# Kernel optimization log

Hardware: AMD Instinct MI355X
Metric: run time of the kernel (lower is better)

## Reference

```python
import jax, jax.numpy as jnp
import numpy as np

D_MODEL = 512
NUM_HEADS = 8
D_K = D_MODEL // NUM_HEADS
LN_EPS = 1e-5


def setup_inputs() -> dict:
    key = jax.random.key(0)
    ks = jax.random.split(key, 11)
    d = D_MODEL
    s = 1.0 / np.sqrt(d)
    return {
        "x": jax.random.normal(ks[0], (4, 2048, d), dtype=jnp.float32),
        "Wq": jax.random.uniform(ks[1], (d, d), jnp.float32, -s, s),
        "bq": jax.random.uniform(ks[2], (d,), jnp.float32, -s, s),
        "Wk": jax.random.uniform(ks[3], (d, d), jnp.float32, -s, s),
        "bk": jax.random.uniform(ks[4], (d,), jnp.float32, -s, s),
        "Wv": jax.random.uniform(ks[5], (d, d), jnp.float32, -s, s),
        "bv": jax.random.uniform(ks[6], (d,), jnp.float32, -s, s),
        "Wo": jax.random.uniform(ks[7], (d, d), jnp.float32, -s, s),
        "bo": jax.random.uniform(ks[8], (d,), jnp.float32, -s, s),
        "gamma": jnp.ones((d,), jnp.float32),
        "beta": jnp.zeros((d,), jnp.float32),
    }


def reference(x, Wq, bq, Wk, bk, Wv, bv, Wo, bo, gamma, beta):
    # x: (B, S, D). Dropout is identity (eval mode).
    B, S, D = x.shape
    H, dk = NUM_HEADS, D_K
    # Linear layers use torch convention: y = x @ W.T + b
    q = (x @ Wq.T + bq).reshape(B, S, H, dk).transpose(0, 2, 1, 3)  # (B,H,S,dk)
    k = (x @ Wk.T + bk).reshape(B, S, H, dk).transpose(0, 2, 1, 3)
    v = (x @ Wv.T + bv).reshape(B, S, H, dk).transpose(0, 2, 1, 3)
    scores = jnp.einsum("bhqd,bhkd->bhqk", q, k) / jnp.sqrt(jnp.float32(dk))
    attn = jax.nn.softmax(scores, axis=-1)
    ctx = jnp.einsum("bhqk,bhkd->bhqd", attn, v)  # (B,H,S,dk)
    ctx = ctx.transpose(0, 2, 1, 3).reshape(B, S, D)
    out = ctx @ Wo.T + bo
    # residual + LayerNorm
    y = x + out
    mu = jnp.mean(y, axis=-1, keepdims=True)
    var = jnp.mean(jnp.square(y - mu), axis=-1, keepdims=True)
    return (y - mu) / jnp.sqrt(var + LN_EPS) * gamma + beta
```

## Files before the change

### kernel.cpp

```cpp
#include <hip/hip_runtime.h>
#include <math.h>

#define D 512
#define NH 8
#define DK 64
#define S 2048
#define BATCH 4
#define N_TOK (BATCH * S)

#define QSCALE 0.18033688f

typedef __bf16 bf16x8 __attribute__((ext_vector_type(8)));
typedef __bf16 bf16x4 __attribute__((ext_vector_type(4)));
typedef float f32x4 __attribute__((ext_vector_type(4)));
typedef unsigned int u32x4 __attribute__((ext_vector_type(4)));

#define AS1 __attribute__((address_space(1)))
#define AS3 __attribute__((address_space(3)))

#define OFF_XB   0
#define OFF_WB   8388608
#define OFF_Q    10485760
#define OFF_K    18874368
#define OFF_VT   27262976
#define OFF_CTX  35651584
#define OFF_FLAG 44040192

static __device__ __forceinline__ bf16x8 ldg8(const __bf16* p) {
    return *(const bf16x8*)p;
}
static __device__ __forceinline__ f32x4 mfma16(bf16x8 a, bf16x8 b, f32x4 c) {
    return __builtin_amdgcn_mfma_f32_16x16x32_bf16(a, b, c, 0, 0, 0);
}
static __device__ __forceinline__ float ldf(const void* p, size_t i, int isf) {
    return isf ? ((const float*)p)[i] : (float)(((const __bf16*)p)[i]);
}
static __device__ __forceinline__ float fexp2(float x) {
#if __has_builtin(__builtin_amdgcn_exp2f)
    return __builtin_amdgcn_exp2f(x);
#else
    return exp2f(x);
#endif
}
static __device__ __forceinline__ unsigned pack_trunc(float e0, float e1) {
    return (__builtin_bit_cast(unsigned, e0) >> 16)
         | (__builtin_bit_cast(unsigned, e1) & 0xFFFF0000u);
}
static __device__ __forceinline__ void gload_lds16(const void* g, void* l) {
    __builtin_amdgcn_global_load_lds((const AS1 char*)g, (AS3 char*)l, 16, 0, 0);
}

__global__ __launch_bounds__(256)
void cvt_kernel(const void* __restrict__ x,  const void* __restrict__ Wq,
                const void* __restrict__ Wk, const void* __restrict__ Wv,
                const void* __restrict__ Wo, __bf16* __restrict__ xb,
                __bf16* __restrict__ Wb, int* __restrict__ flag)
{
    const bf16x8 probe = ldg8((const __bf16*)x + (threadIdx.x & 63) * 8);
    int bad = 0;
#pragma unroll
    for (int j = 0; j < 8; ++j) bad |= !(fabsf((float)probe[j]) <= 64.0f);
    const int isf = __any(bad) ? 1 : 0;
    if (blockIdx.x == 0 && threadIdx.x == 0) *flag = isf;

    const size_t i0 = ((size_t)blockIdx.x * 256 + threadIdx.x) * 8;
    const void* src;
    __bf16* dst;
    size_t off;
    if (i0 < 4194304) {
        src = x; off = i0; dst = xb + i0;
    } else {
        const size_t wrel = i0 - 4194304;
        const size_t w = wrel >> 18;
        src = (w == 0) ? Wq : (w == 1) ? Wk : (w == 2) ? Wv : Wo;
        off = wrel & 262143;
        dst = Wb + wrel;
    }
    bf16x8 r;
    if (isf) {
        const float* f = (const float*)src + off;
#pragma unroll
        for (int j = 0; j < 8; ++j) r[j] = (__bf16)f[j];
    } else {
        r = *(const bf16x8*)((const __bf16*)src + off);
    }
    *(bf16x8*)dst = r;
}

__global__ __launch_bounds__(256)
void qkv_kernel(const __bf16* __restrict__ xb, const __bf16* __restrict__ Wb,
                const void* __restrict__ bq, const void* __restrict__ bk,
                const void* __restrict__ bv, const int* __restrict__ flag,
                __bf16* __restrict__ Q, __bf16* __restrict__ K,
                __bf16* __restrict__ Vt)
{
    __shared__ __align__(16) char smem[32768];

    const int isf = *flag;
    const int tid = threadIdx.x;
    const int w = tid >> 6, l = tid & 63;
    const int lane16 = l & 15, quad = l >> 4;
    const int wm = w >> 1, wn = w & 1;
    const int m0 = blockIdx.x * 128;
    const int by = blockIdx.y;
    const int n0 = by * 128;

    const int cwl = w * 64 + l;
    const int g0 = (cwl & 3) ^ ((cwl >> 3) & 3);
    const __bf16* aS0 = xb + (size_t)(m0 + (cwl >> 2)) * D + g0 * 8;
    const __bf16* aS1 = aS0 + (size_t)64 * D;
    const __bf16* bS0 = Wb + (size_t)(n0 + (cwl >> 2)) * D + g0 * 8;
    const __bf16* bS1 = bS0 + (size_t)64 * D;

    const int sw = (quad ^ ((lane16 >> 1) & 3)) * 16;
    const int aoff = (wm * 64 + lane16) * 64 + sw;
    const int boff = 8192 + (wn * 64 + lane16) * 64 + sw;

    f32x4 acc[4][4];
#pragma unroll
    for (int i = 0; i < 4; ++i)
#pragma unroll
        for (int j = 0; j < 4; ++j) acc[i][j] = (f32x4){0,0,0,0};

    gload_lds16(aS0, smem + w * 1024);
    gload_lds16(aS1, smem + 4096 + w * 1024);
    gload_lds16(bS0, smem + 8192 + w * 1024);
    gload_lds16(bS1, smem + 12288 + w * 1024);

    for (int kt = 0; kt < D / 32; ++kt) {
        __syncthreads();

        const char* bufp = smem + (kt & 1) * 16384;
        if (kt + 1 < D / 32) {
            char* nb = smem + ((kt + 1) & 1) * 16384;
            gload_lds16(aS0 + (kt + 1) * 32, nb + w * 1024);
            gload_lds16(aS1 + (kt + 1) * 32, nb + 4096 + w * 1024);
            gload_lds16(bS0 + (kt + 1) * 32, nb + 8192 + w * 1024);
            gload_lds16(bS1 + (kt + 1) * 32, nb + 12288 + w * 1024);
        }

        bf16x8 af[4], bf[4];
#pragma unroll
        for (int i = 0; i < 4; ++i) af[i] = *(const bf16x8*)(bufp + aoff + i * 1024);
#pragma unroll
        for (int j = 0; j < 4; ++j) bf[j] = *(const bf16x8*)(bufp + boff + j * 1024);
#pragma unroll
        for (int i = 0; i < 4; ++i)
#pragma unroll
            for (int j = 0; j < 4; ++j)
                acc[i][j] = mfma16(af[i], bf[j], acc[i][j]);
    }

    const int which = by >> 2;
    const int h = (by * 2 + wn) & 7;
    const float qs = (which == 0) ? QSCALE : 1.0f;
    const void* bias = (which == 0) ? bq : (which == 1) ? bk : bv;
    float bvv[4];
#pragma unroll
    for (int j = 0; j < 4; ++j)
        bvv[j] = ldf(bias, ((by & 3) * 128 + wn * 64 + 16 * j + lane16) & 511, isf);

    const int bb = m0 >> 11;
    const int ssb = (m0 & (S - 1)) + wm * 64;

    if (which < 2) {
        __bf16* out = ((which == 0) ? Q : K) + ((size_t)(bb * NH + h) * S) * DK;
#pragma unroll
        for (int i = 0; i < 4; ++i)
#pragma unroll
            for (int r = 0; r < 4; ++r) {
                const int ss = ssb + i * 16 + quad * 4 + r;
#pragma unroll
                for (int j = 0; j < 4; ++j)
                    out[(size_t)ss * DK + 16 * j + lane16] =
                        (__bf16)((acc[i][j][r] + bvv[j]) * qs);
            }
    } else {
#pragma unroll
        for (int i = 0; i < 4; ++i)
#pragma unroll
            for (int j = 0; j < 4; ++j) {
                const int dkc = 16 * j + lane16;
                __bf16* vp = Vt + ((size_t)(bb * NH + h) * DK + dkc) * S
                                + ssb + (quad + 4 * (i >> 1)) * 8 + 4 * (i & 1);
                bf16x4 pkt;
#pragma unroll
                for (int r = 0; r < 4; ++r) pkt[r] = (__bf16)(acc[i][j][r] + bvv[j]);
                *(bf16x4*)vp = pkt;
            }
    }
}

__global__ __launch_bounds__(512, 4)
void attn_kernel(const __bf16* __restrict__ Q, const __bf16* __restrict__ K,
                 const __bf16* __restrict__ Vt, __bf16* __restrict__ ctx)
{
    __shared__ __align__(16) char smem[65536];

    const int tid = threadIdx.x;
    const int w = tid >> 6, l = tid & 63;
    const int lane16 = l & 15, quad = l >> 4;
    const int team = w >> 2, tq = w & 3;

    const int lin = blockIdx.x;
    const int xcd = lin & 7;
    const int t = lin >> 3;
    const int bh = xcd * 4 + (t >> 4);
    const int qt = t & 15;
    const int b = bh >> 3, h = bh & 7;
    const size_t bhS = (size_t)bh * S;

    const int cwl = w * 64 + l;
    const int row = cwl >> 3;
    const int g = (cwl & 7) ^ (row & 7);
    const char* kS = (const char*)(K + (bhS + row) * DK) + g * 16;
    const char* vS = (const char*)(Vt + ((size_t)bh * DK + row) * S) + g * 16;

    const int qbase = qt * 128 + tq * 32;
    bf16x8 qa[2][2];
#pragma unroll
    for (int u = 0; u < 2; ++u) {
        const __bf16* Qp = Q + (bhS + qbase + u * 16 + lane16) * DK + quad * 8;
        qa[u][0] = ldg8(Qp);
        qa[u][1] = ldg8(Qp + 32);
    }

    bf16x8 aones;
#pragma unroll
    for (int j = 0; j < 8; ++j) aones[j] = (__bf16)1.0f;

    const int x7 = lane16 & 7;

    f32x4 o[2][4], lacc[2];
#pragma unroll
    for (int u = 0; u < 2; ++u) {
        lacc[u] = (f32x4){0,0,0,0};
#pragma unroll
        for (int tt = 0; tt < 4; ++tt) o[u][tt] = (f32x4){0,0,0,0};
    }

    gload_lds16(kS, smem + w * 1024);
    gload_lds16(vS, smem + 8192 + w * 1024);
    gload_lds16(kS + 8192, smem + 32768 + w * 1024);
    gload_lds16(vS + 128, smem + 32768 + 8192 + w * 1024);

    for (int p = 0; p < S / 128; ++p) {
        __syncthreads();

        const char* kb = smem + (team * 2 + (p & 1)) * 16384;
        const char* vb = kb + 8192;

        if (p + 1 < S / 128) {
            const int ns = (p + 1) & 1;
            const size_t c1 = 2 * p + 2, c2 = 2 * p + 3;
            char* b1 = smem + ns * 16384;
            char* b2 = smem + (2 + ns) * 16384;
            gload_lds16(kS + c1 * 8192, b1 + w * 1024);
            gload_lds16(vS + c1 * 128,  b1 + 8192 + w * 1024);
            gload_lds16(kS + c2 * 8192, b2 + w * 1024);
            gload_lds16(vS + c2 * 128,  b2 + 8192 + w * 1024);
        }

        f32x4 st[2][4];
#pragma unroll
        for (int tt = 0; tt < 4; ++tt) {
            const int base = (tt * 16 + lane16) * 128;
            const bf16x8 kfA = *(const bf16x8*)(kb + base + ((quad ^ x7) * 16));
            const bf16x8 kfB = *(const bf16x8*)(kb + base
                                                + (((quad + 4) ^ x7) * 16));
            __builtin_amdgcn_s_setprio(1);
#pragma unroll
            for (int u = 0; u < 2; ++u) {
                f32x4 z = {0,0,0,0};
                z = mfma16(kfA, qa[u][0], z);
                st[u][tt] = mfma16(kfB, qa[u][1], z);
            }
            __builtin_amdgcn_s_setprio(0);
        }

        bf16x8 bp[2][2];
#pragma unroll
        for (int u = 0; u < 2; ++u) {
            u32x4 u0, u1;
            u0[0] = pack_trunc(fexp2(st[u][0][0]), fexp2(st[u][0][1]));
            u0[1] = pack_trunc(fexp2(st[u][0][2]), fexp2(st[u][0][3]));
            u0[2] = pack_trunc(fexp2(st[u][1][0]), fexp2(st[u][1][1]));
            u0[3] = pack_trunc(fexp2(st[u][1][2]), fexp2(st[u][1][3]));
            u1[0] = pack_trunc(fexp2(st[u][2][0]), fexp2(st[u][2][1]));
            u1[1] = pack_trunc(fexp2(st[u][2][2]), fexp2(st[u][2][3]));
            u1[2] = pack_trunc(fexp2(st[u][3][0]), fexp2(st[u][3][1]));
            u1[3] = pack_trunc(fexp2(st[u][3][2]), fexp2(st[u][3][3]));
            bp[u][0] = __builtin_bit_cast(bf16x8, u0);
            bp[u][1] = __builtin_bit_cast(bf16x8, u1);
        }

#pragma unroll
        for (int tt = 0; tt < 4; ++tt) {
            const int base = (tt * 16 + lane16) * 128;
            const bf16x8 vA = *(const bf16x8*)(vb + base + ((quad ^ x7) * 16));
            const bf16x8 vB = *(const bf16x8*)(vb + base
                                               + (((quad + 4) ^ x7) * 16));
            __builtin_amdgcn_s_setprio(1);
#pragma unroll
            for (int u = 0; u < 2; ++u) {
                o[u][tt] = mfma16(vA, bp[u][0], o[u][tt]);
                o[u][tt] = mfma16(vB, bp[u][1], o[u][tt]);
            }
            __builtin_amdgcn_s_setprio(0);
        }
        __builtin_amdgcn_s_setprio(1);
#pragma unroll
        for (int u = 0; u < 2; ++u) {
            lacc[u] = mfma16(aones, bp[u][0], lacc[u]);
            lacc[u] = mfma16(aones, bp[u][1], lacc[u]);
        }
        __builtin_amdgcn_s_setprio(0);
    }

    __syncthreads();
    if (team == 1) {
        char* obase = smem + tq * 8192;
#pragma unroll
        for (int u = 0; u < 2; ++u)
#pragma unroll
            for (int tt = 0; tt < 4; ++tt)
                *(f32x4*)(obase + (u * 4 + tt) * 1024 + l * 16) = o[u][tt];
        float* lb = (float*)(smem + 32768 + tq * 512 + l * 8);
        lb[0] = lacc[0][0];
        lb[1] = lacc[1][0];
    }
    __syncthreads();
    if (team == 0) {
        const char* obase = smem + tq * 8192;
        const float* lb = (const float*)(smem + 32768 + tq * 512 + l * 8);
#pragma unroll
        for (int u = 0; u < 2; ++u) {
            const float inv = 1.0f / (lacc[u][0] + lb[u]);
            __bf16* cp = ctx + ((size_t)(b * S + qbase + u * 16 + lane16)) * D
                         + h * DK;
#pragma unroll
            for (int tt = 0; tt < 4; ++tt) {
                const f32x4 po = *(const f32x4*)(obase + (u * 4 + tt) * 1024
                                                 + l * 16);
                bf16x4 pkt;
#pragma unroll
                for (int r = 0; r < 4; ++r)
                    pkt[r] = (__bf16)((o[u][tt][r] + po[r]) * inv);
                *(bf16x4*)(cp + tt * 16 + quad * 4) = pkt;
            }
        }
    }
}

__global__ __launch_bounds__(512)
void proj_ln_kernel(const __bf16* __restrict__ ctx, const __bf16* __restrict__ Wb,
                    const void* __restrict__ bo, const __bf16* __restrict__ xb,
                    const void* __restrict__ gamma, const void* __restrict__ beta,
                    const int* __restrict__ flag, void* __restrict__ out)
{
    __shared__ __align__(16) char smem[67584];

    const int isf = *flag;
    const int tid = threadIdx.x;
    const int w = tid >> 6, l = tid & 63;
    const int lane16 = l & 15, quad = l >> 4;
    const int m0 = blockIdx.x * 16;

    const __bf16* Wo = Wb + (size_t)3 * 262144;
    const int cwl = tid;

    const int gA = (cwl & 3) ^ ((cwl >> 3) & 3);
    const __bf16* aS = ctx + (size_t)(m0 + ((cwl & 63) >> 2)) * D + gA * 8;

    const __bf16* bS[4];
#pragma unroll
    for (int c = 0; c < 4; ++c) {
        const int s = c * 512 + cwl;
        const int gB = (s & 3) ^ ((s >> 3) & 3);
        bS[c] = Wo + (size_t)(s >> 2) * D + gB * 8;
    }

    const int sw = (quad ^ ((lane16 >> 1) & 3)) * 16;
    const int aoff = lane16 * 64 + sw;
    const int boff = 1024 + (w * 64 + lane16) * 64 + sw;

    f32x4 acc[4];
#pragma unroll
    for (int j = 0; j < 4; ++j) acc[j] = (f32x4){0,0,0,0};

    if (w == 0) gload_lds16(aS, smem);
#pragma unroll
    for (int c = 0; c < 4; ++c)
        gload_lds16(bS[c], smem + 1024 + c * 8192 + w * 1024);

    for (int kt = 0; kt < D / 32; ++kt) {
        __syncthreads();

        const char* bufp = smem + (kt & 1) * 33792;
        if (kt + 1 < D / 32) {
            char* nb = smem + ((kt + 1) & 1) * 33792;
            if (w == 0) gload_lds16(aS + (kt + 1) * 32, nb);
#pragma unroll
            for (int c = 0; c < 4; ++c)
                gload_lds16(bS[c] + (kt + 1) * 32,
                            nb + 1024 + c * 8192 + w * 1024);
        }

        const bf16x8 af = *(const bf16x8*)(bufp + aoff);
        bf16x8 bf[4];
#pragma unroll
        for (int j = 0; j < 4; ++j) bf[j] = *(const bf16x8*)(bufp + boff + j * 1024);
#pragma unroll
        for (int j = 0; j < 4; ++j)
            acc[j] = mfma16(af, bf[j], acc[j]);
    }

    float bvv[4], gv[4], bev[4];
#pragma unroll
    for (int j = 0; j < 4; ++j) {
        const int col = w * 64 + 16 * j + lane16;
        bvv[j] = ldf(bo, col, isf);
        gv[j]  = ldf(gamma, col, isf);
        bev[j] = ldf(beta, col, isf);
    }

    float v[4][4];
#pragma unroll
    for (int r = 0; r < 4; ++r) {
        const int tok = m0 + quad * 4 + r;
#pragma unroll
        for (int j = 0; j < 4; ++j) {
            const int col = w * 64 + 16 * j + lane16;
            v[r][j] = acc[j][r] + bvv[j] + (float)xb[(size_t)tok * D + col];
        }
    }

#pragma unroll
    for (int r = 0; r < 4; ++r) {
        float s1 = v[r][0] + v[r][1] + v[r][2] + v[r][3];
        float s2 = v[r][0]*v[r][0] + v[r][1]*v[r][1]
                 + v[r][2]*v[r][2] + v[r][3]*v[r][3];
#pragma unroll
        for (int msk = 1; msk < 16; msk <<= 1) {
            s1 += __shfl_xor(s1, msk);
            s2 += __shfl_xor(s2, msk);
        }
        if (lane16 == 0) {
            float* pp = (float*)(smem + ((w * 16 + quad * 4 + r) * 8));
            pp[0] = s1;
            pp[1] = s2;
        }
    }
    __syncthreads();

    if (tid < 16) {
        float s1 = 0.f, s2 = 0.f;
#pragma unroll
        for (int ww = 0; ww < 8; ++ww) {
            const float* pp = (const float*)(smem + ((ww * 16 + tid) * 8));
            s1 += pp[0];
            s2 += pp[1];
        }
        const float mean = s1 * (1.0f / D);
        const float var  = s2 * (1.0f / D) - mean * mean;
        float* st = (float*)(smem + 2048 + tid * 8);
        st[0] = mean;
        st[1] = rsqrtf(var + 1e-5f);
    }
    __syncthreads();

#pragma unroll
    for (int r = 0; r < 4; ++r) {
        const int row = quad * 4 + r;
        const float* st = (const float*)(smem + 2048 + row * 8);
        const float mean = st[0], rstd = st[1];
        const size_t tb = (size_t)(m0 + row) * D;
#pragma unroll
        for (int j = 0; j < 4; ++j) {
            const int col = w * 64 + 16 * j + lane16;
            const float res = (v[r][j] - mean) * rstd * gv[j] + bev[j];
            if (isf) ((float*)out)[tb + col] = res;
            else     ((__bf16*)out)[tb + col] = (__bf16)res;
        }
    }
}

extern "C" void kernel_launch(void* const* d_in, const int* in_sizes, int n_in,
                              void* d_out, int out_size, void* d_ws,
                              size_t ws_size, hipStream_t stream)
{
    const void* x     = d_in[0];
    const void* Wq    = d_in[1];
    const void* bq    = d_in[2];
    const void* Wk    = d_in[3];
    const void* bk    = d_in[4];
    const void* Wv    = d_in[5];
    const void* bv    = d_in[6];
    const void* Wo    = d_in[7];
    const void* bo    = d_in[8];
    const void* gamma = d_in[9];
    const void* beta  = d_in[10];

    char* ws = (char*)d_ws;
    __bf16* xb  = (__bf16*)(ws + OFF_XB);
    __bf16* Wb  = (__bf16*)(ws + OFF_WB);
    __bf16* Qb  = (__bf16*)(ws + OFF_Q);
    __bf16* Kb  = (__bf16*)(ws + OFF_K);
    __bf16* Vtb = (__bf16*)(ws + OFF_VT);
    __bf16* ctx = (__bf16*)(ws + OFF_CTX);
    int*    flag = (int*)(ws + OFF_FLAG);

    cvt_kernel<<<5242880 / (256 * 8), 256, 0, stream>>>(
        x, Wq, Wk, Wv, Wo, xb, Wb, flag);
    qkv_kernel<<<dim3(N_TOK / 128, 12), 256, 0, stream>>>(
        xb, Wb, bq, bk, bv, flag, Qb, Kb, Vtb);
    attn_kernel<<<dim3(512), 512, 0, stream>>>(Qb, Kb, Vtb, ctx);
    proj_ln_kernel<<<dim3(N_TOK / 16), 512, 0, stream>>>(
        ctx, Wb, bo, xb, gamma, beta, flag, d_out);
}
```

Before: 168.2 us.

## Split attention waves over key halves with larger query tiles, drop ones-MFMA row sums

Reorganizes the attention kernel's wave work split: each wave now handles 64 queries (4 MFMA row tiles) over half of each 32-key chunk, instead of 32 queries over the full chunk. Each loaded K/V fragment is reused across more query tiles, and the PV MFMA now takes a single 16-key K-slice per tile. The softmax denominator is accumulated in scalar registers from the packed bf16 probabilities, replacing the extra MFMAs against a ones vector. The price is more registers for Q and O accumulators and a longer multi-stage LDS reduction across four partial sums at the end.

Result: slower. 307.1 us (+82.6%).

```diff
diff --git a/kernel.cpp b/kernel.cpp
--- a/kernel.cpp
+++ b/kernel.cpp
@@ -200,7 +200,7 @@
     const int tid = threadIdx.x;
     const int w = tid >> 6, l = tid & 63;
     const int lane16 = l & 15, quad = l >> 4;
-    const int team = w >> 2, tq = w & 3;
+    const int qg = w & 1, kh = (w >> 1) & 1, team = w >> 2;
 
     const int lin = blockIdx.x;
     const int xcd = lin & 7;
@@ -216,28 +216,25 @@
     const char* kS = (const char*)(K + (bhS + row) * DK) + g * 16;
     const char* vS = (const char*)(Vt + ((size_t)bh * DK + row) * S) + g * 16;
 
-    const int qbase = qt * 128 + tq * 32;
-    bf16x8 qa[2][2];
-#pragma unroll
-    for (int u = 0; u < 2; ++u) {
+    const int qbase = qt * 128 + qg * 64;
+    bf16x8 qa[4][2];
+#pragma unroll
+    for (int u = 0; u < 4; ++u) {
         const __bf16* Qp = Q + (bhS + qbase + u * 16 + lane16) * DK + quad * 8;
         qa[u][0] = ldg8(Qp);
         qa[u][1] = ldg8(Qp + 32);
     }
 
-    bf16x8 aones;
-#pragma unroll
-    for (int j = 0; j < 8; ++j) aones[j] = (__bf16)1.0f;
-
     const int x7 = lane16 & 7;
-
-    f32x4 o[2][4], lacc[2];
-#pragma unroll
-    for (int u = 0; u < 2; ++u) {
-        lacc[u] = (f32x4){0,0,0,0};
+    const int krow0 = kh * 4096 + lane16 * 128;
+    const int vblk = ((kh * 4 + quad) ^ x7) * 16;
+
+    f32x4 o[4][4];
+    float l4[4] = {0.f, 0.f, 0.f, 0.f};
+#pragma unroll
+    for (int u = 0; u < 4; ++u)
 #pragma unroll
         for (int tt = 0; tt < 4; ++tt) o[u][tt] = (f32x4){0,0,0,0};
-    }
 
     gload_lds16(kS, smem + w * 1024);
     gload_lds16(vS, smem + 8192 + w * 1024);
@@ -261,91 +258,116 @@
             gload_lds16(vS + c2 * 128,  b2 + 8192 + w * 1024);
         }
 
-        f32x4 st[2][4];
-#pragma unroll
-        for (int tt = 0; tt < 4; ++tt) {
-            const int base = (tt * 16 + lane16) * 128;
+        u32x4 bw[4];
+#pragma unroll
+        for (int kt2 = 0; kt2 < 2; ++kt2) {
+            const int base = krow0 + kt2 * 2048;
             const bf16x8 kfA = *(const bf16x8*)(kb + base + ((quad ^ x7) * 16));
             const bf16x8 kfB = *(const bf16x8*)(kb + base
                                                 + (((quad + 4) ^ x7) * 16));
+            f32x4 stv[4];
             __builtin_amdgcn_s_setprio(1);
 #pragma unroll
-            for (int u = 0; u < 2; ++u) {
+            for (int u = 0; u < 4; ++u) {
                 f32x4 z = {0,0,0,0};
                 z = mfma16(kfA, qa[u][0], z);
-                st[u][tt] = mfma16(kfB, qa[u][1], z);
+                stv[u] = mfma16(kfB, qa[u][1], z);
             }
             __builtin_amdgcn_s_setprio(0);
-        }
-
-        bf16x8 bp[2][2];
-#pragma unroll
-        for (int u = 0; u < 2; ++u) {
-            u32x4 u0, u1;
-            u0[0] = pack_trunc(fexp2(st[u][0][0]), fexp2(st[u][0][1]));
-            u0[1] = pack_trunc(fexp2(st[u][0][2]), fexp2(st[u][0][3]));
-            u0[2] = pack_trunc(fexp2(st[u][1][0]), fexp2(st[u][1][1]));
-            u0[3] = pack_trunc(fexp2(st[u][1][2]), fexp2(st[u][1][3]));
-            u1[0] = pack_trunc(fexp2(st[u][2][0]), fexp2(st[u][2][1]));
-            u1[1] = pack_trunc(fexp2(st[u][2][2]), fexp2(st[u][2][3]));
-            u1[2] = pack_trunc(fexp2(st[u][3][0]), fexp2(st[u][3][1]));
-            u1[3] = pack_trunc(fexp2(st[u][3][2]), fexp2(st[u][3][3]));
-            bp[u][0] = __builtin_bit_cast(bf16x8, u0);
-            bp[u][1] = __builtin_bit_cast(bf16x8, u1);
-        }
-
-#pragma unroll
-        for (int tt = 0; tt < 4; ++tt) {
-            const int base = (tt * 16 + lane16) * 128;
-            const bf16x8 vA = *(const bf16x8*)(vb + base + ((quad ^ x7) * 16));
-            const bf16x8 vB = *(const bf16x8*)(vb + base
-                                               + (((quad + 4) ^ x7) * 16));
-            __builtin_amdgcn_s_setprio(1);
-#pragma unroll
-            for (int u = 0; u < 2; ++u) {
-                o[u][tt] = mfma16(vA, bp[u][0], o[u][tt]);
-                o[u][tt] = mfma16(vB, bp[u][1], o[u][tt]);
+#pragma unroll
+            for (int u = 0; u < 4; ++u) {
+                const unsigned w0 = pack_trunc(fexp2(stv[u][0]), fexp2(stv[u][1]));
+                const unsigned w1 = pack_trunc(fexp2(stv[u][2]), fexp2(stv[u][3]));
+                bw[u][kt2 * 2]     = w0;
+                bw[u][kt2 * 2 + 1] = w1;
+                l4[u] += __builtin_bit_cast(float, w0 << 16)
+                       + __builtin_bit_cast(float, w0 & 0xFFFF0000u)
+                       + __builtin_bit_cast(float, w1 << 16)
+                       + __builtin_bit_cast(float, w1 & 0xFFFF0000u);
             }
-            __builtin_amdgcn_s_setprio(0);
-        }
+        }
+
+        bf16x8 vA[4];
+#pragma unroll
+        for (int tt = 0; tt < 4; ++tt)
+            vA[tt] = *(const bf16x8*)(vb + (tt * 16 + lane16) * 128 + vblk);
+
         __builtin_amdgcn_s_setprio(1);
 #pragma unroll
-        for (int u = 0; u < 2; ++u) {
-            lacc[u] = mfma16(aones, bp[u][0], lacc[u]);
-            lacc[u] = mfma16(aones, bp[u][1], lacc[u]);
+        for (int u = 0; u < 4; ++u) {
+            const bf16x8 bp = __builtin_bit_cast(bf16x8, bw[u]);
+#pragma unroll
+            for (int tt = 0; tt < 4; ++tt)
+                o[u][tt] = mfma16(vA[tt], bp, o[u][tt]);
         }
         __builtin_amdgcn_s_setprio(0);
     }
 
     __syncthreads();
+#pragma unroll
+    for (int u = 0; u < 4; ++u) {
+        l4[u] += __shfl_xor(l4[u], 16);
+        l4[u] += __shfl_xor(l4[u], 32);
+    }
+    if (quad == 0) {
+        float* lp = (float*)(smem + w * 256 + lane16 * 16);
+#pragma unroll
+        for (int u = 0; u < 4; ++u) lp[u] = l4[u];
+    }
+    __syncthreads();
+    float inv[4];
+    if (team == 0 && kh == 0) {
+#pragma unroll
+        for (int u = 0; u < 4; ++u) {
+            const float s = l4[u]
+                + *(const float*)(smem + (w + 2) * 256 + lane16 * 16 + u * 4)
+                + *(const float*)(smem + (w + 4) * 256 + lane16 * 16 + u * 4)
+                + *(const float*)(smem + (w + 6) * 256 + lane16 * 16 + u * 4);
+            inv[u] = 1.0f / s;
+        }
+    }
+    __syncthreads();
     if (team == 1) {
-        char* obase = smem + tq * 8192;
-#pragma unroll
-        for (int u = 0; u < 2; ++u)
+        char* rg = smem + (qg * 2 + kh) * 16384;
+#pragma unroll
+        for (int u = 0; u < 4; ++u)
 #pragma unroll
             for (int tt = 0; tt < 4; ++tt)
-                *(f32x4*)(obase + (u * 4 + tt) * 1024 + l * 16) = o[u][tt];
-        float* lb = (float*)(smem + 32768 + tq * 512 + l * 8);
-        lb[0] = lacc[0][0];
-        lb[1] = lacc[1][0];
+                *(f32x4*)(rg + (u * 4 + tt) * 1024 + l * 16) = o[u][tt];
     }
     __syncthreads();
     if (team == 0) {
-        const char* obase = smem + tq * 8192;
-        const float* lb = (const float*)(smem + 32768 + tq * 512 + l * 8);
-#pragma unroll
-        for (int u = 0; u < 2; ++u) {
-            const float inv = 1.0f / (lacc[u][0] + lb[u]);
+        const char* rg = smem + (qg * 2 + kh) * 16384;
+#pragma unroll
+        for (int u = 0; u < 4; ++u)
+#pragma unroll
+            for (int tt = 0; tt < 4; ++tt)
+                o[u][tt] += *(const f32x4*)(rg + (u * 4 + tt) * 1024 + l * 16);
+    }
+    __syncthreads();
+    if (team == 0 && kh == 1) {
+        char* rg = smem + qg * 16384;
+#pragma unroll
+        for (int u = 0; u < 4; ++u)
+#pragma unroll
+            for (int tt = 0; tt < 4; ++tt)
+                *(f32x4*)(rg + (u * 4 + tt) * 1024 + l * 16) = o[u][tt];
+    }
+    __syncthreads();
+    if (team == 0 && kh == 0) {
+        const char* rg = smem + qg * 16384;
+#pragma unroll
+        for (int u = 0; u < 4; ++u) {
             __bf16* cp = ctx + ((size_t)(b * S + qbase + u * 16 + lane16)) * D
                          + h * DK;
 #pragma unroll
             for (int tt = 0; tt < 4; ++tt) {
-                const f32x4 po = *(const f32x4*)(obase + (u * 4 + tt) * 1024
+                const f32x4 po = *(const f32x4*)(rg + (u * 4 + tt) * 1024
                                                  + l * 16);
                 bf16x4 pkt;
 #pragma unroll
                 for (int r = 0; r < 4; ++r)
-                    pkt[r] = (__bf16)((o[u][tt][r] + po[r]) * inv);
+                    pkt[r] = (__bf16)((o[u][tt][r] + po[r]) * inv[u]);
                 *(bf16x4*)(cp + tt * 16 + quad * 4) = pkt;
             }
         }
```
